# Optimization experiments

Hardware: AMD Instinct MI355X
Metric: run time of the kernel (lower is better)

Reference implementation:

```python
import jax, jax.numpy as jnp
import numpy as np

N_NODES = 50000
D = 512
N_EDGES = 1600000

def setup_inputs() -> dict:
    key = jax.random.key(0)
    ks = jax.random.split(key, 5)
    x = jax.random.normal(ks[0], (N_NODES, D), dtype=jnp.float32)
    W = jax.random.normal(ks[1], (D, D), dtype=jnp.float32) * (1.0 / np.sqrt(D))
    b = jnp.zeros((D,), dtype=jnp.float32)
    edge_weight = jax.random.uniform(ks[2], (N_EDGES,), dtype=jnp.float32)
    edge_src = jax.random.randint(ks[3], (N_EDGES,), 0, N_NODES, dtype=jnp.int32)
    edge_dst = jax.random.randint(ks[4], (N_EDGES,), 0, N_NODES, dtype=jnp.int32)
    return {"x": x, "W": W, "b": b, "edge_weight": edge_weight,
            "edge_src": edge_src, "edge_dst": edge_dst}

def reference(x, W, b, edge_weight, edge_src, edge_dst):
    # GraphConvolution: support = x @ W; out = spmm(adj, support) + b
    support = x @ W                                  # [N, D] dense GEMM
    msgs = support[edge_src] * edge_weight[:, None]  # gather + scale [E, D]
    agg = jax.ops.segment_sum(msgs, edge_dst, num_segments=x.shape[0])  # [N, D]
    gc_out = agg + b
    # GCN2: relu then residual
    return jax.nn.relu(gc_out) + x
```

## Files before the change

kernel.cpp:

```cpp
#include <hip/hip_runtime.h>

#define N_NODES 50000
#define DIM 512
#define KCAT 1024
#define N_EDGES 1600000
#define CAP 96

typedef __attribute__((ext_vector_type(8))) short short8;
typedef __attribute__((ext_vector_type(8))) unsigned short ushort8;
typedef __attribute__((ext_vector_type(4))) float floatx4;

__device__ __forceinline__ unsigned short f2bf(float v) {
    unsigned u = __float_as_uint(v);
    unsigned r = u + 0x7FFF + ((u >> 16) & 1);
    return (unsigned short)(r >> 16);
}
__device__ __forceinline__ float bf2f(unsigned short h) {
    return __uint_as_float((unsigned)h << 16);
}
__device__ __forceinline__ void stage16(const char* g, char* l) {
    __builtin_amdgcn_global_load_lds((const __attribute__((address_space(1))) void*)g,
                                     (__attribute__((address_space(3))) void*)l, 16, 0, 0);
}

__global__ __launch_bounds__(256) void convert_x(const float* __restrict__ x,
                                                 unsigned short* __restrict__ xcat) {
    const int t = blockIdx.x * 256 + threadIdx.x;
    if (t >= N_NODES * 64) return;
    const int row = t >> 6;
    const int kc = t & 63;
    const int blk = kc >> 3;
    const int c = kc & 7;
    const int cSw = c ^ (row & 7);

    const float4 v0 = *(const float4*)&x[row * DIM + kc * 8];
    const float4 v1 = *(const float4*)&x[row * DIM + kc * 8 + 4];
    float v[8] = {v0.x, v0.y, v0.z, v0.w, v1.x, v1.y, v1.z, v1.w};
    unsigned short h[8], l[8];
#pragma unroll
    for (int j = 0; j < 8; j++) {
        h[j] = f2bf(v[j]);
        l[j] = f2bf(v[j] - bf2f(h[j]));
    }
    const int o = row * KCAT + blk * 64 + cSw * 8;
    *(short8*)&xcat[o] = *(short8*)h;
    *(short8*)&xcat[o + DIM] = *(short8*)l;
}

__global__ __launch_bounds__(256) void convert_w(const float* __restrict__ W,
                                                 unsigned short* __restrict__ wcat) {
    const int t = blockIdx.x * 256 + threadIdx.x;
    if (t >= DIM * 64) return;
    const int n = t >> 6;
    const int kc = t & 63;
    const int blk = kc >> 3;
    const int c = kc & 7;
    const int cSw = c ^ (n & 7);

    unsigned short h[8];
#pragma unroll
    for (int j = 0; j < 8; j++) h[j] = f2bf(W[(kc * 8 + j) * DIM + n]);
    const int o = n * KCAT + blk * 64 + cSw * 8;
    *(short8*)&wcat[o] = *(short8*)h;
    *(short8*)&wcat[o + DIM] = *(short8*)h;
}

__global__ __launch_bounds__(256, 3) void gemm_cat(const unsigned short* __restrict__ A,
                                                   const unsigned short* __restrict__ B,
                                                   unsigned short* __restrict__ Cb, int M) {
    __shared__ __align__(128) char smem[32768];

    const int tid = threadIdx.x;
    const int row0 = blockIdx.y * 128;
    const int col0 = blockIdx.x * 128;

    int srow[4], schk[4];
#pragma unroll
    for (int i = 0; i < 4; i++) {
        const int q = i * 256 + tid;
        srow[i] = q >> 3;
        schk[i] = q & 7;
    }

    const int l = tid & 63;
    const int w = tid >> 6;
    const int wm = w & 1, wn = w >> 1;
    const int lrow = l & 15;
    const int kg = l >> 4;
    const int s = l & 7;

    int offA[4][2], offB[4][2];
#pragma unroll
    for (int mt = 0; mt < 4; mt++)
#pragma unroll
        for (int h = 0; h < 2; h++) {
            const int chunk = (kg + 4 * h) ^ s;
            offA[mt][h] = (wm * 64 + mt * 16 + lrow) * 128 + chunk * 16;
            offB[mt][h] = 16384 + (wn * 64 + mt * 16 + lrow) * 128 + chunk * 16;
        }

    floatx4 acc[4][4];
#pragma unroll
    for (int i = 0; i < 4; i++)
#pragma unroll
        for (int j = 0; j < 4; j++) acc[i][j] = (floatx4)(0.f);

    const char* A8 = (const char*)A;
    const char* B8 = (const char*)B;

    for (int kblk = 0; kblk < 16; kblk++) {
        __syncthreads();
#pragma unroll
        for (int i = 0; i < 4; i++) {
            const int q16 = (i * 256 + tid) * 16;
            const size_t ga = (size_t)min(row0 + srow[i], M - 1) * (KCAT * 2)
                              + kblk * 128 + schk[i] * 16;
            const size_t gb = (size_t)(col0 + srow[i]) * (KCAT * 2)
                              + kblk * 128 + schk[i] * 16;
            stage16(A8 + ga, smem + q16);
            stage16(B8 + gb, smem + 16384 + q16);
        }
        __syncthreads();

#pragma unroll
        for (int h = 0; h < 2; h++) {
            short8 bf[4];
#pragma unroll
            for (int nt = 0; nt < 4; nt++) bf[nt] = *(const short8*)(smem + offB[nt][h]);
#pragma unroll
            for (int mt = 0; mt < 4; mt++) {
                const short8 af = *(const short8*)(smem + offA[mt][h]);
#pragma unroll
                for (int nt = 0; nt < 4; nt++)
                    acc[mt][nt] = __builtin_amdgcn_mfma_f32_16x16x32_bf16(
                        af, bf[nt], acc[mt][nt], 0, 0, 0);
            }
        }
    }

    const int crow0 = row0 + wm * 64;
    const int ccol0 = col0 + wn * 64;
#pragma unroll
    for (int mt = 0; mt < 4; mt++) {
        const int rbase = crow0 + mt * 16 + kg * 4;
#pragma unroll
        for (int nt = 0; nt < 4; nt++) {
            const int cc = ccol0 + nt * 16 + lrow;
#pragma unroll
            for (int r = 0; r < 4; r++) {
                const int gr = rbase + r;
                if (gr < M) Cb[(size_t)gr * DIM + cc] = f2bf(acc[mt][nt][r]);
            }
        }
    }
}

__global__ __launch_bounds__(256) void gcn_build_edges(const int* __restrict__ esrc,
                                                       const int* __restrict__ edst,
                                                       const float* __restrict__ ew,
                                                       int* __restrict__ cursor,
                                                       uint2* __restrict__ table) {
    const int e = blockIdx.x * 256 + threadIdx.x;
    if (e >= N_EDGES) return;
    const int d = edst[e];
    const int pos = atomicAdd(&cursor[d], 1);
    if (pos < CAP) {
        table[d * CAP + pos] = make_uint2((unsigned)esrc[e], __float_as_uint(ew[e]));
    }
}

__global__ __launch_bounds__(64) void gcn_aggregate(const unsigned short* __restrict__ sup,
                                                    const int* __restrict__ cursor,
                                                    const uint2* __restrict__ table,
                                                    const unsigned short* __restrict__ xcat,
                                                    const float* __restrict__ b,
                                                    float* __restrict__ out) {
    const int n = blockIdx.x;
    const int tid = threadIdx.x;
    const int c = tid * 8;

    __shared__ uint2 s_e[CAP];
    const int deg = min(cursor[n], CAP);
    if (tid < deg) s_e[tid] = table[n * CAP + tid];
    if (tid + 64 < deg) s_e[tid + 64] = table[n * CAP + tid + 64];
    __syncthreads();

    float acc[8];
#pragma unroll
    for (int j = 0; j < 8; j++) acc[j] = 0.f;

#pragma unroll 4
    for (int i = 0; i < deg; i++) {
        const uint2 e = s_e[i];
        const float wt = __uint_as_float(e.y);
        const ushort8 v = *(const ushort8*)&sup[(size_t)e.x * DIM + c];
#pragma unroll
        for (int j = 0; j < 8; j++) acc[j] = fmaf(wt, bf2f(v[j]), acc[j]);
    }

    const int xoff = n * KCAT + (tid >> 3) * 64 + (((tid & 7) ^ (n & 7)) * 8);
    const ushort8 xb = *(const ushort8*)&xcat[xoff];
    const float4 b0 = *(const float4*)&b[c];
    const float4 b1 = *(const float4*)&b[c + 4];
    const float bb[8] = {b0.x, b0.y, b0.z, b0.w, b1.x, b1.y, b1.z, b1.w};
    floatx4 o0, o1;
    float o[8];
#pragma unroll
    for (int j = 0; j < 8; j++) o[j] = fmaxf(acc[j] + bb[j], 0.f) + bf2f(xb[j]);
    o0.x = o[0]; o0.y = o[1]; o0.z = o[2]; o0.w = o[3];
    o1.x = o[4]; o1.y = o[5]; o1.z = o[6]; o1.w = o[7];
    __builtin_nontemporal_store(o0, (floatx4*)&out[n * DIM + c]);
    __builtin_nontemporal_store(o1, (floatx4*)&out[n * DIM + c + 4]);
}

extern "C" void kernel_launch(void* const* d_in, const int* in_sizes, int n_in,
                              void* d_out, int out_size, void* d_ws, size_t ws_size,
                              hipStream_t stream) {
    const float* x = (const float*)d_in[0];
    const float* W = (const float*)d_in[1];
    const float* b = (const float*)d_in[2];
    const float* ew = (const float*)d_in[3];
    const int* esrc = (const int*)d_in[4];
    const int* edst = (const int*)d_in[5];
    float* out = (float*)d_out;

    char* ws = (char*)d_ws;
    size_t off = 0;
    unsigned short* support = (unsigned short*)(ws + off); off += (size_t)N_NODES * DIM * 2;
    int* cursor = (int*)(ws + off);                   off += (size_t)N_NODES * 4;
    uint2* table = (uint2*)(ws + off);                off += (size_t)N_NODES * CAP * 8;
    unsigned short* xcat = (unsigned short*)(ws + off); off += (size_t)N_NODES * KCAT * 2;
    unsigned short* wcat = (unsigned short*)(ws + off); off += (size_t)DIM * KCAT * 2;

    (void)hipMemsetAsync(cursor, 0, (size_t)N_NODES * sizeof(int), stream);

    convert_w<<<(DIM * 64 + 255) / 256, 256, 0, stream>>>(W, wcat);
    convert_x<<<(N_NODES * 64 + 255) / 256, 256, 0, stream>>>(x, xcat);

    gcn_build_edges<<<(N_EDGES + 255) / 256, 256, 0, stream>>>(esrc, edst, ew,
                                                               cursor, table);

    dim3 gemm_grid(DIM / 128, (N_NODES + 127) / 128);
    gemm_cat<<<gemm_grid, 256, 0, stream>>>(xcat, wcat, support, N_NODES);

    gcn_aggregate<<<N_NODES, 64, 0, stream>>>(support, cursor, table, xcat, b, out);
}
```

Measured before the change: 627.1 us.

## Split GEMM and aggregation into two column halves and stage GEMM output through LDS

The GEMM and the sparse aggregation now run in two passes over 256-column halves of the feature dimension. The aim is to keep each half of the support matrix (about 25 MB of bf16) resident in cache while the random gathers read it. The GEMM epilogue also writes through LDS, so each row goes out as a coalesced 16-byte store instead of scattered 2-byte stores. In exchange, each aggregation thread now gathers only 8 bytes per edge, and the edge table and cursor are read twice, once per pass.

```diff
diff --git a/kernel.cpp b/kernel.cpp
--- a/kernel.cpp
+++ b/kernel.cpp
@@ -8,6 +8,7 @@
 
 typedef __attribute__((ext_vector_type(8))) short short8;
 typedef __attribute__((ext_vector_type(8))) unsigned short ushort8;
+typedef __attribute__((ext_vector_type(4))) unsigned short ushort4v;
 typedef __attribute__((ext_vector_type(4))) float floatx4;
 
 __device__ __forceinline__ unsigned short f2bf(float v) {
@@ -67,12 +68,13 @@
 
 __global__ __launch_bounds__(256, 3) void gemm_cat(const unsigned short* __restrict__ A,
                                                    const unsigned short* __restrict__ B,
-                                                   unsigned short* __restrict__ Cb, int M) {
+                                                   unsigned short* __restrict__ Cb,
+                                                   int M, int colbase) {
     __shared__ __align__(128) char smem[32768];
 
     const int tid = threadIdx.x;
     const int row0 = blockIdx.y * 128;
-    const int col0 = blockIdx.x * 128;
+    const int col0 = (colbase + blockIdx.x) * 128;
 
     int srow[4], schk[4];
 #pragma unroll
@@ -138,19 +140,30 @@
         }
     }
 
+    __syncthreads();
+    char* my = smem + w * 8192;
+#pragma unroll
+    for (int mt = 0; mt < 4; mt++)
+#pragma unroll
+        for (int nt = 0; nt < 4; nt++)
+#pragma unroll
+            for (int r = 0; r < 4; r++) {
+                const int rr = mt * 16 + kg * 4 + r;
+                const int cc = nt * 16 + lrow;
+                *(unsigned short*)(my + rr * 128 + cc * 2) = f2bf(acc[mt][nt][r]);
+            }
+    __syncthreads();
+
     const int crow0 = row0 + wm * 64;
     const int ccol0 = col0 + wn * 64;
 #pragma unroll
-    for (int mt = 0; mt < 4; mt++) {
-        const int rbase = crow0 + mt * 16 + kg * 4;
-#pragma unroll
-        for (int nt = 0; nt < 4; nt++) {
-            const int cc = ccol0 + nt * 16 + lrow;
-#pragma unroll
-            for (int r = 0; r < 4; r++) {
-                const int gr = rbase + r;
-                if (gr < M) Cb[(size_t)gr * DIM + cc] = f2bf(acc[mt][nt][r]);
-            }
+    for (int t = 0; t < 8; t++) {
+        const int rr = t * 8 + (l >> 3);
+        const int cc = (l & 7) * 8;
+        const int gr = crow0 + rr;
+        if (gr < M) {
+            const ushort8 val = *(const ushort8*)(my + t * 1024 + l * 16);
+            *(ushort8*)&Cb[(size_t)gr * DIM + ccol0 + cc] = val;
         }
     }
 }
@@ -174,43 +187,40 @@
                                                     const uint2* __restrict__ table,
                                                     const unsigned short* __restrict__ xcat,
                                                     const float* __restrict__ b,
-                                                    float* __restrict__ out) {
+                                                    float* __restrict__ out,
+                                                    int pass) {
     const int n = blockIdx.x;
-    const int tid = threadIdx.x;
-    const int c = tid * 8;
+    const int j = threadIdx.x;
+    const int cbase = pass * 256 + j * 4;
 
     __shared__ uint2 s_e[CAP];
     const int deg = min(cursor[n], CAP);
-    if (tid < deg) s_e[tid] = table[n * CAP + tid];
-    if (tid + 64 < deg) s_e[tid + 64] = table[n * CAP + tid + 64];
+    if (j < deg) s_e[j] = table[n * CAP + j];
+    if (j + 64 < deg) s_e[j + 64] = table[n * CAP + j + 64];
     __syncthreads();
 
-    float acc[8];
-#pragma unroll
-    for (int j = 0; j < 8; j++) acc[j] = 0.f;
-
+    float acc[4] = {0.f, 0.f, 0.f, 0.f};
 #pragma unroll 4
     for (int i = 0; i < deg; i++) {
         const uint2 e = s_e[i];
         const float wt = __uint_as_float(e.y);
-        const ushort8 v = *(const ushort8*)&sup[(size_t)e.x * DIM + c];
-#pragma unroll
-        for (int j = 0; j < 8; j++) acc[j] = fmaf(wt, bf2f(v[j]), acc[j]);
-    }
-
-    const int xoff = n * KCAT + (tid >> 3) * 64 + (((tid & 7) ^ (n & 7)) * 8);
-    const ushort8 xb = *(const ushort8*)&xcat[xoff];
-    const float4 b0 = *(const float4*)&b[c];
-    const float4 b1 = *(const float4*)&b[c + 4];
-    const float bb[8] = {b0.x, b0.y, b0.z, b0.w, b1.x, b1.y, b1.z, b1.w};
-    floatx4 o0, o1;
-    float o[8];
-#pragma unroll
-    for (int j = 0; j < 8; j++) o[j] = fmaxf(acc[j] + bb[j], 0.f) + bf2f(xb[j]);
-    o0.x = o[0]; o0.y = o[1]; o0.z = o[2]; o0.w = o[3];
-    o1.x = o[4]; o1.y = o[5]; o1.z = o[6]; o1.w = o[7];
-    __builtin_nontemporal_store(o0, (floatx4*)&out[n * DIM + c]);
-    __builtin_nontemporal_store(o1, (floatx4*)&out[n * DIM + c + 4]);
+        const ushort4v v = *(const ushort4v*)&sup[(size_t)e.x * DIM + cbase];
+#pragma unroll
+        for (int q = 0; q < 4; q++) acc[q] = fmaf(wt, bf2f(v[q]), acc[q]);
+    }
+
+    const int blk = (pass * 4) + (j >> 4);
+    const int chunk = ((j & 15) >> 1) ^ (n & 7);
+    const int xoff = n * KCAT + blk * 64 + chunk * 8 + (j & 1) * 4;
+    const ushort4v xb = *(const ushort4v*)&xcat[xoff];
+
+    const float4 bb = *(const float4*)&b[cbase];
+    floatx4 o;
+    o.x = fmaxf(acc[0] + bb.x, 0.f) + bf2f(xb[0]);
+    o.y = fmaxf(acc[1] + bb.y, 0.f) + bf2f(xb[1]);
+    o.z = fmaxf(acc[2] + bb.z, 0.f) + bf2f(xb[2]);
+    o.w = fmaxf(acc[3] + bb.w, 0.f) + bf2f(xb[3]);
+    __builtin_nontemporal_store(o, (floatx4*)&out[n * DIM + cbase]);
 }
 
 extern "C" void kernel_launch(void* const* d_in, const int* in_sizes, int n_in,
@@ -240,8 +250,9 @@
     gcn_build_edges<<<(N_EDGES + 255) / 256, 256, 0, stream>>>(esrc, edst, ew,
                                                                cursor, table);
 
-    dim3 gemm_grid(DIM / 128, (N_NODES + 127) / 128);
-    gemm_cat<<<gemm_grid, 256, 0, stream>>>(xcat, wcat, support, N_NODES);
-
-    gcn_aggregate<<<N_NODES, 64, 0, stream>>>(support, cursor, table, xcat, b, out);
-}
+    dim3 ggrid(2, (N_NODES + 127) / 128);
+    gemm_cat<<<ggrid, 256, 0, stream>>>(xcat, wcat, support, N_NODES, 0);
+    gcn_aggregate<<<N_NODES, 64, 0, stream>>>(support, cursor, table, xcat, b, out, 0);
+    gemm_cat<<<ggrid, 256, 0, stream>>>(xcat, wcat, support, N_NODES, 2);
+    gcn_aggregate<<<N_NODES, 64, 0, stream>>>(support, cursor, table, xcat, b, out, 1);
+}
```

New measurement: 630.9 us. No clear change (+0.6%).

## Aggregate neighbors before the GEMM and fuse bias, ReLU and residual into its epilogue

Applied to the files above, without the earlier changes.

Uses associativity to compute the sparse aggregation A·x first, in two 256-column passes over bf16 x. It then runs the dense GEMM (A·x)·W with bias, ReLU and the residual fused into the GEMM epilogue, removing the separate support buffer and the final elementwise pass. Edge entries are packed into 32 bits: a 17-bit source index and a 15-bit fixed-point weight. The packing shrinks the table and the shared-memory traffic, but it assumes weights lie in [0,1] and lowers their precision. The new epilogue issues scalar, strided loads and stores, and the aggregation now writes a hi/lo bf16 pair per row, which doubles its output size.

```diff
diff --git a/kernel.cpp b/kernel.cpp
--- a/kernel.cpp
+++ b/kernel.cpp
@@ -8,6 +8,7 @@
 
 typedef __attribute__((ext_vector_type(8))) short short8;
 typedef __attribute__((ext_vector_type(8))) unsigned short ushort8;
+typedef __attribute__((ext_vector_type(4))) unsigned short ushort4v;
 typedef __attribute__((ext_vector_type(4))) float floatx4;
 
 __device__ __forceinline__ unsigned short f2bf(float v) {
@@ -24,27 +25,16 @@
 }
 
 __global__ __launch_bounds__(256) void convert_x(const float* __restrict__ x,
-                                                 unsigned short* __restrict__ xcat) {
+                                                 unsigned short* __restrict__ xh) {
     const int t = blockIdx.x * 256 + threadIdx.x;
     if (t >= N_NODES * 64) return;
-    const int row = t >> 6;
-    const int kc = t & 63;
-    const int blk = kc >> 3;
-    const int c = kc & 7;
-    const int cSw = c ^ (row & 7);
-
-    const float4 v0 = *(const float4*)&x[row * DIM + kc * 8];
-    const float4 v1 = *(const float4*)&x[row * DIM + kc * 8 + 4];
-    float v[8] = {v0.x, v0.y, v0.z, v0.w, v1.x, v1.y, v1.z, v1.w};
-    unsigned short h[8], l[8];
-#pragma unroll
-    for (int j = 0; j < 8; j++) {
-        h[j] = f2bf(v[j]);
-        l[j] = f2bf(v[j] - bf2f(h[j]));
-    }
-    const int o = row * KCAT + blk * 64 + cSw * 8;
-    *(short8*)&xcat[o] = *(short8*)h;
-    *(short8*)&xcat[o + DIM] = *(short8*)l;
+    const float4 v0 = *(const float4*)&x[t * 8];
+    const float4 v1 = *(const float4*)&x[t * 8 + 4];
+    const float v[8] = {v0.x, v0.y, v0.z, v0.w, v1.x, v1.y, v1.z, v1.w};
+    unsigned short h[8];
+#pragma unroll
+    for (int j = 0; j < 8; j++) h[j] = f2bf(v[j]);
+    *(short8*)&xh[t * 8] = *(short8*)h;
 }
 
 __global__ __launch_bounds__(256) void convert_w(const float* __restrict__ W,
@@ -65,9 +55,64 @@
     *(short8*)&wcat[o + DIM] = *(short8*)h;
 }
 
-__global__ __launch_bounds__(256, 3) void gemm_cat(const unsigned short* __restrict__ A,
-                                                   const unsigned short* __restrict__ B,
-                                                   unsigned short* __restrict__ Cb, int M) {
+__global__ __launch_bounds__(256) void gcn_build_edges(const int* __restrict__ esrc,
+                                                       const int* __restrict__ edst,
+                                                       const float* __restrict__ ew,
+                                                       int* __restrict__ cursor,
+                                                       unsigned* __restrict__ table) {
+    const int e = blockIdx.x * 256 + threadIdx.x;
+    if (e >= N_EDGES) return;
+    const int d = edst[e];
+    const int pos = atomicAdd(&cursor[d], 1);
+    if (pos < CAP) {
+        const unsigned wq = (unsigned)(ew[e] * 32767.0f + 0.5f) & 0x7FFF;
+        table[d * CAP + pos] = ((unsigned)esrc[e] << 15) | wq;
+    }
+}
+
+__global__ __launch_bounds__(64) void gcn_aggregate(const unsigned short* __restrict__ xh,
+                                                    const int* __restrict__ cursor,
+                                                    const unsigned* __restrict__ table,
+                                                    unsigned short* __restrict__ aggcat,
+                                                    int pass) {
+    const int n = blockIdx.x;
+    const int j = threadIdx.x;
+    const int cbase = pass * 256 + j * 4;
+
+    __shared__ unsigned s_e[CAP];
+    const int deg = min(cursor[n], CAP);
+    if (j < deg) s_e[j] = table[n * CAP + j];
+    if (j + 64 < deg) s_e[j + 64] = table[n * CAP + j + 64];
+    __syncthreads();
+
+    float acc[4] = {0.f, 0.f, 0.f, 0.f};
+#pragma unroll 4
+    for (int i = 0; i < deg; i++) {
+        const unsigned p = s_e[i];
+        const float wt = (float)(p & 0x7FFF) * (1.0f / 32767.0f);
+        const ushort4v v = *(const ushort4v*)&xh[(size_t)(p >> 15) * DIM + cbase];
+#pragma unroll
+        for (int q = 0; q < 4; q++) acc[q] = fmaf(wt, bf2f(v[q]), acc[q]);
+    }
+
+    const int blk = pass * 4 + (j >> 4);
+    const int cSw = ((j >> 1) & 7) ^ (n & 7);
+    const int o = n * KCAT + blk * 64 + cSw * 8 + (j & 1) * 4;
+    unsigned short hq[4], lq[4];
+#pragma unroll
+    for (int q = 0; q < 4; q++) {
+        hq[q] = f2bf(acc[q]);
+        lq[q] = f2bf(acc[q] - bf2f(hq[q]));
+    }
+    *(ushort4v*)&aggcat[o] = *(ushort4v*)hq;
+    *(ushort4v*)&aggcat[o + DIM] = *(ushort4v*)lq;
+}
+
+__global__ __launch_bounds__(256, 3) void gemm_fused(const unsigned short* __restrict__ A,
+                                                     const unsigned short* __restrict__ B,
+                                                     const unsigned short* __restrict__ xh,
+                                                     const float* __restrict__ bias,
+                                                     float* __restrict__ out, int M) {
     __shared__ __align__(128) char smem[32768];
 
     const int tid = threadIdx.x;
@@ -140,6 +185,9 @@
 
     const int crow0 = row0 + wm * 64;
     const int ccol0 = col0 + wn * 64;
+    float bb[4];
+#pragma unroll
+    for (int nt = 0; nt < 4; nt++) bb[nt] = bias[ccol0 + nt * 16 + lrow];
 #pragma unroll
     for (int mt = 0; mt < 4; mt++) {
         const int rbase = crow0 + mt * 16 + kg * 4;
@@ -149,68 +197,14 @@
 #pragma unroll
             for (int r = 0; r < 4; r++) {
                 const int gr = rbase + r;
-                if (gr < M) Cb[(size_t)gr * DIM + cc] = f2bf(acc[mt][nt][r]);
+                if (gr < M) {
+                    const float res = bf2f(xh[(size_t)gr * DIM + cc]);
+                    out[(size_t)gr * DIM + cc] =
+                        fmaxf(acc[mt][nt][r] + bb[nt], 0.f) + res;
+                }
             }
         }
     }
-}
-
-__global__ __launch_bounds__(256) void gcn_build_edges(const int* __restrict__ esrc,
-                                                       const int* __restrict__ edst,
-                                                       const float* __restrict__ ew,
-                                                       int* __restrict__ cursor,
-                                                       uint2* __restrict__ table) {
-    const int e = blockIdx.x * 256 + threadIdx.x;
-    if (e >= N_EDGES) return;
-    const int d = edst[e];
-    const int pos = atomicAdd(&cursor[d], 1);
-    if (pos < CAP) {
-        table[d * CAP + pos] = make_uint2((unsigned)esrc[e], __float_as_uint(ew[e]));
-    }
-}
-
-__global__ __launch_bounds__(64) void gcn_aggregate(const unsigned short* __restrict__ sup,
-                                                    const int* __restrict__ cursor,
-                                                    const uint2* __restrict__ table,
-                                                    const unsigned short* __restrict__ xcat,
-                                                    const float* __restrict__ b,
-                                                    float* __restrict__ out) {
-    const int n = blockIdx.x;
-    const int tid = threadIdx.x;
-    const int c = tid * 8;
-
-    __shared__ uint2 s_e[CAP];
-    const int deg = min(cursor[n], CAP);
-    if (tid < deg) s_e[tid] = table[n * CAP + tid];
-    if (tid + 64 < deg) s_e[tid + 64] = table[n * CAP + tid + 64];
-    __syncthreads();
-
-    float acc[8];
-#pragma unroll
-    for (int j = 0; j < 8; j++) acc[j] = 0.f;
-
-#pragma unroll 4
-    for (int i = 0; i < deg; i++) {
-        const uint2 e = s_e[i];
-        const float wt = __uint_as_float(e.y);
-        const ushort8 v = *(const ushort8*)&sup[(size_t)e.x * DIM + c];
-#pragma unroll
-        for (int j = 0; j < 8; j++) acc[j] = fmaf(wt, bf2f(v[j]), acc[j]);
-    }
-
-    const int xoff = n * KCAT + (tid >> 3) * 64 + (((tid & 7) ^ (n & 7)) * 8);
-    const ushort8 xb = *(const ushort8*)&xcat[xoff];
-    const float4 b0 = *(const float4*)&b[c];
-    const float4 b1 = *(const float4*)&b[c + 4];
-    const float bb[8] = {b0.x, b0.y, b0.z, b0.w, b1.x, b1.y, b1.z, b1.w};
-    floatx4 o0, o1;
-    float o[8];
-#pragma unroll
-    for (int j = 0; j < 8; j++) o[j] = fmaxf(acc[j] + bb[j], 0.f) + bf2f(xb[j]);
-    o0.x = o[0]; o0.y = o[1]; o0.z = o[2]; o0.w = o[3];
-    o1.x = o[4]; o1.y = o[5]; o1.z = o[6]; o1.w = o[7];
-    __builtin_nontemporal_store(o0, (floatx4*)&out[n * DIM + c]);
-    __builtin_nontemporal_store(o1, (floatx4*)&out[n * DIM + c + 4]);
 }
 
 extern "C" void kernel_launch(void* const* d_in, const int* in_sizes, int n_in,
@@ -226,22 +220,23 @@
 
     char* ws = (char*)d_ws;
     size_t off = 0;
-    unsigned short* support = (unsigned short*)(ws + off); off += (size_t)N_NODES * DIM * 2;
-    int* cursor = (int*)(ws + off);                   off += (size_t)N_NODES * 4;
-    uint2* table = (uint2*)(ws + off);                off += (size_t)N_NODES * CAP * 8;
-    unsigned short* xcat = (unsigned short*)(ws + off); off += (size_t)N_NODES * KCAT * 2;
-    unsigned short* wcat = (unsigned short*)(ws + off); off += (size_t)DIM * KCAT * 2;
+    unsigned short* xh = (unsigned short*)(ws + off);     off += (size_t)N_NODES * DIM * 2;
+    int* cursor = (int*)(ws + off);                       off += (size_t)N_NODES * 4;
+    unsigned* table = (unsigned*)(ws + off);              off += (size_t)N_NODES * CAP * 4;
+    unsigned short* aggcat = (unsigned short*)(ws + off); off += (size_t)N_NODES * KCAT * 2;
+    unsigned short* wcat = (unsigned short*)(ws + off);   off += (size_t)DIM * KCAT * 2;
 
     (void)hipMemsetAsync(cursor, 0, (size_t)N_NODES * sizeof(int), stream);
 
     convert_w<<<(DIM * 64 + 255) / 256, 256, 0, stream>>>(W, wcat);
-    convert_x<<<(N_NODES * 64 + 255) / 256, 256, 0, stream>>>(x, xcat);
+    convert_x<<<(N_NODES * 64 + 255) / 256, 256, 0, stream>>>(x, xh);
 
     gcn_build_edges<<<(N_EDGES + 255) / 256, 256, 0, stream>>>(esrc, edst, ew,
                                                                cursor, table);
 
-    dim3 gemm_grid(DIM / 128, (N_NODES + 127) / 128);
-    gemm_cat<<<gemm_grid, 256, 0, stream>>>(xcat, wcat, support, N_NODES);
-
-    gcn_aggregate<<<N_NODES, 64, 0, stream>>>(support, cursor, table, xcat, b, out);
-}
+    gcn_aggregate<<<N_NODES, 64, 0, stream>>>(xh, cursor, table, aggcat, 0);
+    gcn_aggregate<<<N_NODES, 64, 0, stream>>>(xh, cursor, table, aggcat, 1);
+
+    dim3 ggrid(DIM / 128, (N_NODES + 127) / 128);
+    gemm_fused<<<ggrid, 256, 0, stream>>>(aggcat, wcat, xh, b, out, N_NODES);
+}
```

Result: no change. 634.9 us (+1.2%).
